# Performance work log

Hardware: AMD Instinct MI355X
Metric: run time of the kernel (lower is better)

Reference implementation:

```python
import jax, jax.numpy as jnp
import numpy as np

DIM = 2048
CTX_DIM = 4096
NUM_HEADS = 16
HEAD_DIM = DIM // NUM_HEADS
EPS = 1e-6


def _rms_norm(x, weight, eps=EPS):
    # RMSNorm over last dim with learned weight (native dtype path for fp32)
    var = jnp.mean(jnp.square(x), axis=-1, keepdims=True)
    return x * jax.lax.rsqrt(var + eps) * weight


def setup_inputs() -> dict:
    key = jax.random.key(0)
    ks = jax.random.split(key, 12)
    B, L, S = 1, 8192, 512
    sd_q = 1.0 / np.sqrt(DIM)
    sd_c = 1.0 / np.sqrt(CTX_DIM)
    return {
        "x": jax.random.normal(ks[0], (B, L, DIM), dtype=jnp.float32),
        "context": jax.random.normal(ks[1], (B, S, CTX_DIM), dtype=jnp.float32),
        "Wq": jax.random.normal(ks[2], (DIM, DIM), dtype=jnp.float32) * sd_q,
        "bq": jax.random.normal(ks[3], (DIM,), dtype=jnp.float32) * 0.01,
        "Wk": jax.random.normal(ks[4], (CTX_DIM, DIM), dtype=jnp.float32) * sd_c,
        "bk": jax.random.normal(ks[5], (DIM,), dtype=jnp.float32) * 0.01,
        "Wv": jax.random.normal(ks[6], (CTX_DIM, DIM), dtype=jnp.float32) * sd_c,
        "bv": jax.random.normal(ks[7], (DIM,), dtype=jnp.float32) * 0.01,
        "Wo": jax.random.normal(ks[8], (DIM, DIM), dtype=jnp.float32) * sd_q,
        "bo": jax.random.normal(ks[9], (DIM,), dtype=jnp.float32) * 0.01,
        "g_q": jnp.ones((DIM,), dtype=jnp.float32),
        "g_k": jnp.ones((DIM,), dtype=jnp.float32),
    }


def reference(x, context, Wq, bq, Wk, bk, Wv, bv, Wo, bo, g_q, g_k):
    B, L, C = x.shape
    S = context.shape[1]
    # QKV projections + RMSNorm on Q,K (over full model dim, pre head split)
    q = _rms_norm(x @ Wq + bq, g_q)           # [B, L, C]
    k = _rms_norm(context @ Wk + bk, g_k)     # [B, S, C]
    v = context @ Wv + bv                     # [B, S, C]
    # split heads
    q = q.reshape(B, L, NUM_HEADS, HEAD_DIM)
    k = k.reshape(B, S, NUM_HEADS, HEAD_DIM)
    v = v.reshape(B, S, NUM_HEADS, HEAD_DIM)
    # non-causal SDPA
    scale = 1.0 / np.sqrt(HEAD_DIM)
    scores = jnp.einsum("blhd,bshd->bhls", q, k) * scale
    probs = jax.nn.softmax(scores, axis=-1)
    attn = jnp.einsum("bhls,bshd->blhd", probs, v).reshape(B, L, C)
    return attn @ Wo + bo
```

## Files before the change

kernel.cpp:

```cpp
#include <hip/hip_runtime.h>
#include <hip/hip_bf16.h>
#include <stdint.h>

#define L_SEQ 8192
#define S_SEQ 512
#define DIM   2048
#define CTX   4096
#define NH    16
#define HD    128

typedef __bf16 bf16_t;
typedef bf16_t bf16x8 __attribute__((ext_vector_type(8)));
typedef float  f32x4_t __attribute__((ext_vector_type(4)));
typedef float  f32x16_t __attribute__((ext_vector_type(16)));

__device__ __forceinline__ ushort f2b(float f) {
  union { float f; uint32_t u; } v; v.f = f;
  uint32_t u = v.u;
  uint32_t r = (u + 0x7fffu + ((u >> 16) & 1u)) >> 16;
  return (ushort)r;
}
__device__ __forceinline__ uint32_t pk2(float a, float b) {
  return (uint32_t)f2b(a) | ((uint32_t)f2b(b) << 16);
}
__device__ __forceinline__ float b2f(ushort u) {
  union { uint32_t u; float f; } v; v.u = ((uint32_t)u) << 16;
  return v.f;
}
__device__ __forceinline__ void gll16(const ushort* g, ushort* l) {
  __builtin_amdgcn_global_load_lds((const __attribute__((address_space(1))) void*)g,
                                   (__attribute__((address_space(3))) void*)l, 16, 0, 0);
}

__global__ __launch_bounds__(256) void k_cast(const float* __restrict__ in,
                                              ushort* __restrict__ out) {
  const size_t i = ((size_t)blockIdx.x * 256 + threadIdx.x) * 8;
  float4 a = *(const float4*)(in + i);
  float4 b = *(const float4*)(in + i + 4);
  uint4 r;
  r.x = pk2(a.x, a.y); r.y = pk2(a.z, a.w);
  r.z = pk2(b.x, b.y); r.w = pk2(b.z, b.w);
  *(uint4*)(out + i) = r;
}

__global__ __launch_bounds__(256) void k_tcast(const float* __restrict__ src,
                                               ushort* __restrict__ dst, int K, int N) {
  __shared__ float t[32][33];
  int tx = threadIdx.x, ty = threadIdx.y;
  int n0 = blockIdx.x * 32, k0 = blockIdx.y * 32;
#pragma unroll
  for (int i = 0; i < 4; i++)
    t[ty + 8 * i][tx] = src[(size_t)(k0 + ty + 8 * i) * N + n0 + tx];
  __syncthreads();
#pragma unroll
  for (int i = 0; i < 4; i++)
    dst[(size_t)(n0 + ty + 8 * i) * K + k0 + tx] = f2b(t[tx][ty + 8 * i]);
}

__global__ __launch_bounds__(256) void k_rmsnorm(const ushort* __restrict__ in,
                                                 ushort* __restrict__ out,
                                                 const float* __restrict__ g, float scale) {
  const int row = blockIdx.x, tid = threadIdx.x;
  uint4 v = *(const uint4*)(in + (size_t)row * DIM + tid * 8);
  const uint32_t* vu = (const uint32_t*)&v;
  float f[8];
#pragma unroll
  for (int i = 0; i < 4; i++) {
    f[2 * i]     = b2f((ushort)(vu[i] & 0xffffu));
    f[2 * i + 1] = b2f((ushort)(vu[i] >> 16));
  }
  float s = 0.f;
#pragma unroll
  for (int i = 0; i < 8; i++) s += f[i] * f[i];
#pragma unroll
  for (int off = 32; off; off >>= 1) s += __shfl_down(s, off);
  __shared__ float wsum[4];
  __shared__ float rtot;
  if ((tid & 63) == 0) wsum[tid >> 6] = s;
  __syncthreads();
  if (tid == 0)
    rtot = rsqrtf((wsum[0] + wsum[1] + wsum[2] + wsum[3]) * (1.0f / DIM) + 1e-6f);
  __syncthreads();
  const float rms = rtot * scale;
  const float* gp = g + tid * 8;
  float4 g0 = *(const float4*)gp, g1 = *(const float4*)(gp + 4);
  ushort r[8];
  r[0] = f2b(f[0] * rms * g0.x); r[1] = f2b(f[1] * rms * g0.y);
  r[2] = f2b(f[2] * rms * g0.z); r[3] = f2b(f[3] * rms * g0.w);
  r[4] = f2b(f[4] * rms * g1.x); r[5] = f2b(f[5] * rms * g1.y);
  r[6] = f2b(f[6] * rms * g1.z); r[7] = f2b(f[7] * rms * g1.w);
  *(uint4*)(out + (size_t)row * DIM + tid * 8) = *(uint4*)r;
}

template <int OUT_MODE>
__global__ __launch_bounds__(512, 2) void k_gemm256(const ushort* __restrict__ A,
                                                    const ushort* __restrict__ Bt,
                                                    const float* __restrict__ bias,
                                                    void* __restrict__ outp,
                                                    int M, int N, int K) {
  __shared__ __align__(16) ushort lds[65536];
  const int tid = threadIdx.x;
  const int l = tid & 63, wid = tid >> 6;
  const int wm = wid >> 2, wn = wid & 3;
  const int lr = l & 15, lq = l >> 4;

  const int nwg = gridDim.x * gridDim.y;
  const int bid = blockIdx.y * gridDim.x + blockIdx.x;
  const int swz = (bid & 7) * (nwg >> 3) + (bid >> 3);
  const int m0 = (swz / gridDim.x) * 256, n0 = (swz % gridDim.x) * 256;

  f32x4_t acc[8][4];
#pragma unroll
  for (int i = 0; i < 8; i++)
#pragma unroll
    for (int j = 0; j < 4; j++) acc[i][j] = f32x4_t{0.f, 0.f, 0.f, 0.f};

  const int srow = l >> 3;
  const int schunk = ((l & 7) ^ (srow & 7)) * 8;
  auto stage = [&](int buf, int tile, int mat, int h) {
    const ushort* gp = mat ? Bt : A;
    const int rn0 = mat ? n0 : m0;
    const size_t r0 = (size_t)(rn0 + h * 128 + wid * 8 + srow);
    const ushort* g0 = gp + r0 * K + tile * 64 + schunk;
    ushort* l0 = &lds[buf * 32768 + mat * 16384 + (h * 128 + wid * 8) * 64];
    gll16(g0, l0);
    gll16(g0 + (size_t)64 * K, l0 + 64 * 64);
  };

  auto rdA = [&](int buf, int mf, int ks) -> bf16x8 {
    const int R = wm * 128 + mf * 16 + lr;
    return *(const bf16x8*)(&lds[buf * 32768 + R * 64 + (((ks * 4 + lq) ^ (R & 7)) * 8)]);
  };
  auto rdB = [&](int buf, int nf, int ks) -> bf16x8 {
    const int R = wn * 64 + nf * 16 + lr;
    return *(const bf16x8*)(&lds[buf * 32768 + 16384 + R * 64 + (((ks * 4 + lq) ^ (R & 7)) * 8)]);
  };

  const int NT = K >> 6;
  stage(0, 0, 0, 0); stage(0, 0, 0, 1); stage(0, 0, 1, 0); stage(0, 0, 1, 1);

  bf16x8 a[4][2], a2[4][2], b[2][2], b2[2][2];
  for (int kt = 0; kt < NT; kt++) {
    const int cur = kt & 1, nxt = cur ^ 1;
    const bool pf = (kt + 1 < NT);
    if (pf) { stage(nxt, kt + 1, 0, 0); asm volatile("s_waitcnt vmcnt(2)" ::: "memory"); }
    else    { asm volatile("s_waitcnt vmcnt(0)" ::: "memory"); }
    __builtin_amdgcn_sched_barrier(0);
    __builtin_amdgcn_s_barrier();
    __builtin_amdgcn_sched_barrier(0);
#pragma unroll
    for (int mf = 0; mf < 4; mf++) { a[mf][0] = rdA(cur, mf, 0); a[mf][1] = rdA(cur, mf, 1); }
#pragma unroll
    for (int nf = 0; nf < 2; nf++) { b[nf][0] = rdB(cur, nf, 0); b[nf][1] = rdB(cur, nf, 1); }
    __builtin_amdgcn_s_setprio(1);
#pragma unroll
    for (int mf = 0; mf < 4; mf++)
#pragma unroll
      for (int nf = 0; nf < 2; nf++) {
        acc[mf][nf] = __builtin_amdgcn_mfma_f32_16x16x32_bf16(a[mf][0], b[nf][0], acc[mf][nf], 0, 0, 0);
        acc[mf][nf] = __builtin_amdgcn_mfma_f32_16x16x32_bf16(a[mf][1], b[nf][1], acc[mf][nf], 0, 0, 0);
      }
    __builtin_amdgcn_s_setprio(0);
    __builtin_amdgcn_sched_barrier(0);
    __builtin_amdgcn_s_barrier();
    __builtin_amdgcn_sched_barrier(0);
#pragma unroll
    for (int mf = 0; mf < 4; mf++) { a2[mf][0] = rdA(cur, mf + 4, 0); a2[mf][1] = rdA(cur, mf + 4, 1); }
    if (pf) stage(nxt, kt + 1, 0, 1);
    __builtin_amdgcn_sched_barrier(0);
    __builtin_amdgcn_s_barrier();
    __builtin_amdgcn_sched_barrier(0);
    __builtin_amdgcn_s_setprio(1);
#pragma unroll
    for (int mf = 0; mf < 4; mf++)
#pragma unroll
      for (int nf = 0; nf < 2; nf++) {
        acc[mf + 4][nf] = __builtin_amdgcn_mfma_f32_16x16x32_bf16(a2[mf][0], b[nf][0], acc[mf + 4][nf], 0, 0, 0);
        acc[mf + 4][nf] = __builtin_amdgcn_mfma_f32_16x16x32_bf16(a2[mf][1], b[nf][1], acc[mf + 4][nf], 0, 0, 0);
      }
    __builtin_amdgcn_s_setprio(0);
    __builtin_amdgcn_sched_barrier(0);
    __builtin_amdgcn_s_barrier();
    __builtin_amdgcn_sched_barrier(0);
#pragma unroll
    for (int nf = 0; nf < 2; nf++) { b2[nf][0] = rdB(cur, nf + 2, 0); b2[nf][1] = rdB(cur, nf + 2, 1); }
    if (pf) stage(nxt, kt + 1, 1, 0);
    __builtin_amdgcn_sched_barrier(0);
    __builtin_amdgcn_s_barrier();
    __builtin_amdgcn_sched_barrier(0);
    __builtin_amdgcn_s_setprio(1);
#pragma unroll
    for (int mf = 0; mf < 4; mf++)
#pragma unroll
      for (int nf = 0; nf < 2; nf++) {
        acc[mf + 4][nf + 2] = __builtin_amdgcn_mfma_f32_16x16x32_bf16(a2[mf][0], b2[nf][0], acc[mf + 4][nf + 2], 0, 0, 0);
        acc[mf + 4][nf + 2] = __builtin_amdgcn_mfma_f32_16x16x32_bf16(a2[mf][1], b2[nf][1], acc[mf + 4][nf + 2], 0, 0, 0);
      }
    __builtin_amdgcn_s_setprio(0);
    __builtin_amdgcn_sched_barrier(0);
    __builtin_amdgcn_s_barrier();
    __builtin_amdgcn_sched_barrier(0);
#pragma unroll
    for (int mf = 0; mf < 4; mf++) { a[mf][0] = rdA(cur, mf, 0); a[mf][1] = rdA(cur, mf, 1); }
    if (pf) stage(nxt, kt + 1, 1, 1);
    __builtin_amdgcn_sched_barrier(0);
    __builtin_amdgcn_s_barrier();
    __builtin_amdgcn_sched_barrier(0);
    __builtin_amdgcn_s_setprio(1);
#pragma unroll
    for (int mf = 0; mf < 4; mf++)
#pragma unroll
      for (int nf = 0; nf < 2; nf++) {
        acc[mf][nf + 2] = __builtin_amdgcn_mfma_f32_16x16x32_bf16(a[mf][0], b2[nf][0], acc[mf][nf + 2], 0, 0, 0);
        acc[mf][nf + 2] = __builtin_amdgcn_mfma_f32_16x16x32_bf16(a[mf][1], b2[nf][1], acc[mf][nf + 2], 0, 0, 0);
      }
    __builtin_amdgcn_s_setprio(0);
    __builtin_amdgcn_sched_barrier(0);
    __builtin_amdgcn_s_barrier();
    __builtin_amdgcn_sched_barrier(0);
  }

#pragma unroll
  for (int nf = 0; nf < 4; nf++) {
    const int col = n0 + wn * 64 + nf * 16 + lr;
    const float bv = bias[col];
#pragma unroll
    for (int mf = 0; mf < 8; mf++) {
#pragma unroll
      for (int r = 0; r < 4; r++) {
        const int row = m0 + wm * 128 + mf * 16 + lq * 4 + r;
        const float v = acc[mf][nf][r] + bv;
        if constexpr (OUT_MODE == 0)
          ((float*)outp)[(size_t)row * N + col] = v;
        else
          ((ushort*)outp)[(size_t)row * N + col] = f2b(v);
      }
    }
  }
}

template <int OUT_MODE>
__global__ __launch_bounds__(256) void k_gemm_bt(const ushort* __restrict__ A,
                                                 const ushort* __restrict__ Bt,
                                                 const float* __restrict__ bias,
                                                 const float* __restrict__ bias2,
                                                 void* __restrict__ outp,
                                                 void* __restrict__ outp2,
                                                 int M, int N, int K) {
  __shared__ __align__(16) ushort As[2 * 128 * 32];
  __shared__ __align__(16) ushort Bs[2 * 128 * 32];
  const int tid = threadIdx.x;
  const int l = tid & 63, wid = tid >> 6;
  const int wr = wid >> 1, wc = wid & 1;
  const int lr = l & 15, lq = l >> 4;

  const int nwg = gridDim.x * gridDim.y;
  const int bid = blockIdx.y * gridDim.x + blockIdx.x;
  const int swz = (bid & 7) * (nwg >> 3) + (bid >> 3);
  const int m0 = (swz / gridDim.x) * 128, n0 = (swz % gridDim.x) * 128;

  f32x4_t acc[4][4];
#pragma unroll
  for (int i = 0; i < 4; i++)
#pragma unroll
    for (int j = 0; j < 4; j++) acc[i][j] = f32x4_t{0.f, 0.f, 0.f, 0.f};

  const int srow = l >> 2;
  const int scol = (l & 3) * 8;
  const ushort* ga0 = A  + (size_t)(m0 + wid * 16 + srow) * K + scol;
  const ushort* ga1 = A  + (size_t)(m0 + (4 + wid) * 16 + srow) * K + scol;
  const ushort* gb0 = Bt + (size_t)(n0 + wid * 16 + srow) * K + scol;
  const ushort* gb1 = Bt + (size_t)(n0 + (4 + wid) * 16 + srow) * K + scol;

  auto stageAB = [&](int buf, int kt) {
    const int ko = kt * 32;
    gll16(ga0 + ko, &As[buf * 4096 + wid * 512]);
    gll16(ga1 + ko, &As[buf * 4096 + (4 + wid) * 512]);
    gll16(gb0 + ko, &Bs[buf * 4096 + wid * 512]);
    gll16(gb1 + ko, &Bs[buf * 4096 + (4 + wid) * 512]);
  };

  const int NT = K >> 5;
  stageAB(0, 0);
  for (int kt = 0; kt < NT; kt++) {
    const int cur = kt & 1;
    const bool pf = (kt + 1 < NT);
    if (pf) { stageAB(cur ^ 1, kt + 1); asm volatile("s_waitcnt vmcnt(4)" ::: "memory"); }
    else    { asm volatile("s_waitcnt vmcnt(0)" ::: "memory"); }
    __builtin_amdgcn_sched_barrier(0);
    __builtin_amdgcn_s_barrier();
    __builtin_amdgcn_sched_barrier(0);

    bf16x8 af[4], bfr[4];
#pragma unroll
    for (int mi = 0; mi < 4; mi++)
      af[mi] = *(const bf16x8*)(&As[cur * 4096 + (wr * 64 + mi * 16 + lr) * 32 + lq * 8]);
#pragma unroll
    for (int ni = 0; ni < 4; ni++)
      bfr[ni] = *(const bf16x8*)(&Bs[cur * 4096 + (wc * 64 + ni * 16 + lr) * 32 + lq * 8]);
#pragma unroll
    for (int mi = 0; mi < 4; mi++)
#pragma unroll
      for (int ni = 0; ni < 4; ni++)
        acc[mi][ni] = __builtin_amdgcn_mfma_f32_16x16x32_bf16(af[mi], bfr[ni], acc[mi][ni], 0, 0, 0);
    __builtin_amdgcn_sched_barrier(0);
    __builtin_amdgcn_s_barrier();
    __builtin_amdgcn_sched_barrier(0);
  }

#pragma unroll
  for (int mi = 0; mi < 4; mi++) {
#pragma unroll
    for (int ni = 0; ni < 4; ni++) {
      const int col = n0 + wc * 64 + ni * 16 + lr;
      float bv;
      if constexpr (OUT_MODE == 3) bv = (col < DIM) ? bias[col] : bias2[col - DIM];
      else bv = bias[col];
#pragma unroll
      for (int r = 0; r < 4; r++) {
        const int row = m0 + wr * 64 + mi * 16 + lq * 4 + r;
        const float v = acc[mi][ni][r] + bv;
        if constexpr (OUT_MODE == 0)
          ((float*)outp)[(size_t)row * N + col] = v;
        else if constexpr (OUT_MODE == 1)
          ((ushort*)outp)[(size_t)row * N + col] = f2b(v);
        else {
          if (col < DIM) ((ushort*)outp)[(size_t)row * DIM + col] = f2b(v);
          else ((ushort*)outp2)[(size_t)(col - DIM) * M + row] = f2b(v);
        }
      }
    }
  }
}

__global__ __launch_bounds__(256) void k_attn(const ushort* __restrict__ Qb,
                                              const ushort* __restrict__ Kb,
                                              const ushort* __restrict__ Vt,
                                              ushort* __restrict__ Ob) {
  __shared__ __align__(16) ushort smem[16384];
  ushort* Ks = smem;
  ushort* Vs = smem + 64 * 128;

  const int tid = threadIdx.x;
  const int l = tid & 63, wid = tid >> 6;
  const int lo = l & 31, hi = l >> 5;

  const int bid = blockIdx.x;
  const int swz = (bid & 7) * 128 + (bid >> 3);
  const int h = swz >> 6;
  const int q0 = (swz & 63) * 128 + wid * 32;

  bf16x8 qf[8];
  {
    const ushort* qp = Qb + (size_t)(q0 + lo) * DIM + h * HD + hi * 8;
#pragma unroll
    for (int ds = 0; ds < 8; ds++) qf[ds] = *(const bf16x8*)(qp + ds * 16);
  }

  f32x16_t o[4] = {};
  float m_run = -1e30f, l_run = 0.f;

  for (int kvb = 0; kvb < S_SEQ / 64; kvb++) {
    __syncthreads();
#pragma unroll
    for (int i = 0; i < 4; i++) {
      const int c = i * 256 + tid, row = c >> 4, cs = c & 15;
      gll16(Kb + (size_t)(kvb * 64 + row) * DIM + h * HD + ((cs ^ (row & 7)) * 8),
            Ks + c * 8);
    }
#pragma unroll
    for (int i = 0; i < 4; i++) {
      const int c = i * 256 + tid, row = c >> 3, cs = c & 7;
      gll16(Vt + (size_t)(h * HD + row) * S_SEQ + kvb * 64 + ((cs ^ (row & 7)) * 8),
            Vs + c * 8);
    }
    __syncthreads();

    f32x16_t sA = {}, sB = {};
#pragma unroll
    for (int ds = 0; ds < 8; ds++) {
      const int ch = ((hi + ds * 2) ^ (lo & 7)) * 8;
      bf16x8 kA = *(const bf16x8*)(Ks + lo * 128 + ch);
      bf16x8 kB = *(const bf16x8*)(Ks + (32 + lo) * 128 + ch);
      sA = __builtin_amdgcn_mfma_f32_32x32x16_bf16(kA, qf[ds], sA, 0, 0, 0);
      sB = __builtin_amdgcn_mfma_f32_32x32x16_bf16(kB, qf[ds], sB, 0, 0, 0);
    }

    float p[32];
#pragma unroll
    for (int i = 0; i < 16; i++) { p[i] = sA[i]; p[16 + i] = sB[i]; }
    float pm = p[0];
#pragma unroll
    for (int i = 1; i < 32; i++) pm = fmaxf(pm, p[i]);
    pm = fmaxf(pm, __shfl_xor(pm, 32));
    const float mn = fmaxf(m_run, pm);
    const float corr = __expf(m_run - mn);
    m_run = mn;
    float ps = 0.f;
#pragma unroll
    for (int i = 0; i < 32; i++) { p[i] = __expf(p[i] - mn); ps += p[i]; }
    ps += __shfl_xor(ps, 32);
    l_run = l_run * corr + ps;
#pragma unroll
    for (int nt = 0; nt < 4; nt++) o[nt] *= corr;

    uint32_t c[16];
#pragma unroll
    for (int j = 0; j < 16; j++) c[j] = pk2(p[2 * j], p[2 * j + 1]);
    bf16x8 pf[4];
#pragma unroll
    for (int s = 0; s < 4; s++) {
      const uint32_t ca = c[4 * s], cb = c[4 * s + 1], cc = c[4 * s + 2], cd = c[4 * s + 3];
      const uint32_t sa = __shfl_xor(ca, 32), sb = __shfl_xor(cb, 32);
      const uint32_t sc = __shfl_xor(cc, 32), sd = __shfl_xor(cd, 32);
      union { uint32_t u[4]; bf16x8 v; } f;
      f.u[0] = hi ? sc : ca; f.u[1] = hi ? sd : cb;
      f.u[2] = hi ? cc : sa; f.u[3] = hi ? cd : sb;
      pf[s] = f.v;
    }

#pragma unroll
    for (int nt = 0; nt < 4; nt++) {
      const int vrow = nt * 32 + lo;
#pragma unroll
      for (int s = 0; s < 4; s++) {
        bf16x8 vf = *(const bf16x8*)(Vs + vrow * 64 + (((s * 2 + hi) ^ (lo & 7)) * 8));
        o[nt] = __builtin_amdgcn_mfma_f32_32x32x16_bf16(vf, pf[s], o[nt], 0, 0, 0);
      }
    }
  }

  const float inv = 1.0f / l_run;
#pragma unroll
  for (int nt = 0; nt < 4; nt++) o[nt] *= inv;

  __syncthreads();
  float* tb = (float*)smem + wid * (32 * 33);
  const int q2 = l >> 1, dh = (l & 1) * 16;
#pragma unroll
  for (int nt = 0; nt < 4; nt++) {
#pragma unroll
    for (int r = 0; r < 16; r++)
      tb[lo * 33 + ((r & 3) + 8 * (r >> 2) + 4 * hi)] = o[nt][r];
    asm volatile("s_waitcnt lgkmcnt(0)" ::: "memory");
    __builtin_amdgcn_sched_barrier(0);
    ushort tmp[16];
#pragma unroll
    for (int j = 0; j < 16; j++) tmp[j] = f2b(tb[q2 * 33 + dh + j]);
    asm volatile("s_waitcnt lgkmcnt(0)" ::: "memory");
    __builtin_amdgcn_sched_barrier(0);
    const size_t oaddr = (size_t)(q0 + q2) * DIM + h * HD + nt * 32 + dh;
    *(uint4*)(Ob + oaddr) = *(uint4*)tmp;
    *(uint4*)(Ob + oaddr + 8) = *(uint4*)(tmp + 8);
  }
}

extern "C" void kernel_launch(void* const* d_in, const int* in_sizes, int n_in,
                              void* d_out, int out_size, void* d_ws, size_t ws_size,
                              hipStream_t stream) {
  const float* x   = (const float*)d_in[0];
  const float* ctx = (const float*)d_in[1];
  const float* Wq  = (const float*)d_in[2];
  const float* bq  = (const float*)d_in[3];
  const float* Wk  = (const float*)d_in[4];
  const float* bk  = (const float*)d_in[5];
  const float* Wv  = (const float*)d_in[6];
  const float* bv  = (const float*)d_in[7];
  const float* Wo  = (const float*)d_in[8];
  const float* bo  = (const float*)d_in[9];
  const float* gq  = (const float*)d_in[10];
  const float* gk  = (const float*)d_in[11];

  char* ws = (char*)d_ws;
  ushort* wqt   = (ushort*)(ws);
  ushort* wkt   = (ushort*)(ws + 8388608);
  ushort* wvt   = (ushort*)(ws + 25165824);
  ushort* wot   = (ushort*)(ws + 41943040);
  ushort* qb    = (ushort*)(ws + 50331648);
  ushort* kb    = (ushort*)(ws + 83886080);
  ushort* vt    = (ushort*)(ws + 85983232);
  ushort* xb    = (ushort*)(ws + 88080384);
  ushort* ctxb  = (ushort*)(ws + 88080384);
  ushort* qraw  = (ushort*)(ws + 121634816);
  ushort* kraw  = (ushort*)(ws + 121634816);
  ushort* attnb = (ushort*)(ws + 121634816);

  k_cast<<<L_SEQ * DIM / 8 / 256, 256, 0, stream>>>(x, xb);
  k_tcast<<<dim3(DIM / 32, DIM / 32), dim3(32, 8), 0, stream>>>(Wq, wqt, DIM, DIM);
  k_tcast<<<dim3(DIM / 32, CTX / 32), dim3(32, 8), 0, stream>>>(Wk, wkt, CTX, DIM);
  k_tcast<<<dim3(DIM / 32, CTX / 32), dim3(32, 8), 0, stream>>>(Wv, wvt, CTX, DIM);
  k_tcast<<<dim3(DIM / 32, DIM / 32), dim3(32, 8), 0, stream>>>(Wo, wot, DIM, DIM);

  k_gemm256<1><<<dim3(DIM / 256, L_SEQ / 256), 512, 0, stream>>>(xb, wqt, bq, qraw, L_SEQ, DIM, DIM);
  k_cast<<<S_SEQ * CTX / 8 / 256, 256, 0, stream>>>(ctx, ctxb);
  k_rmsnorm<<<L_SEQ, 256, 0, stream>>>(qraw, qb, gq, 0.08838834764831843f);
  k_gemm_bt<3><<<dim3(2 * DIM / 128, S_SEQ / 128), 256, 0, stream>>>(ctxb, wkt, bk, bv, kraw, vt, S_SEQ, 2 * DIM, CTX);
  k_rmsnorm<<<S_SEQ, 256, 0, stream>>>(kraw, kb, gk, 1.0f);
  k_attn<<<L_SEQ / 128 * NH, 256, 0, stream>>>(qb, kb, vt, attnb);
  k_gemm256<0><<<dim3(DIM / 256, L_SEQ / 256), 512, 0, stream>>>(attnb, wot, bo, d_out, L_SEQ, DIM, DIM);
}
```

Measured before the change: 355.5 us.

## Specialize KV projection GEMM with 128x64 tiles, 4-stage pipeline, swizzled LDS

```diff
diff --git a/kernel.cpp b/kernel.cpp
--- a/kernel.cpp
+++ b/kernel.cpp
@@ -239,70 +239,74 @@
   }
 }
 
-template <int OUT_MODE>
-__global__ __launch_bounds__(256) void k_gemm_bt(const ushort* __restrict__ A,
-                                                 const ushort* __restrict__ Bt,
-                                                 const float* __restrict__ bias,
-                                                 const float* __restrict__ bias2,
-                                                 void* __restrict__ outp,
-                                                 void* __restrict__ outp2,
-                                                 int M, int N, int K) {
-  __shared__ __align__(16) ushort As[2 * 128 * 32];
-  __shared__ __align__(16) ushort Bs[2 * 128 * 32];
+__global__ __launch_bounds__(256) void k_gemmkv(const ushort* __restrict__ A,
+                                                const ushort* __restrict__ Bt,
+                                                const float* __restrict__ biasK,
+                                                const float* __restrict__ biasV,
+                                                ushort* __restrict__ outK,
+                                                ushort* __restrict__ outVt) {
+  __shared__ __align__(16) ushort As[4][128 * 32];
+  __shared__ __align__(16) ushort Bs[4][64 * 32];
   const int tid = threadIdx.x;
   const int l = tid & 63, wid = tid >> 6;
   const int wr = wid >> 1, wc = wid & 1;
   const int lr = l & 15, lq = l >> 4;
-
-  const int nwg = gridDim.x * gridDim.y;
-  const int bid = blockIdx.y * gridDim.x + blockIdx.x;
-  const int swz = (bid & 7) * (nwg >> 3) + (bid >> 3);
-  const int m0 = (swz / gridDim.x) * 128, n0 = (swz % gridDim.x) * 128;
-
-  f32x4_t acc[4][4];
+  const int K = CTX, M = S_SEQ;
+
+  const int bid = blockIdx.x;
+  const int swz = (bid & 7) * 32 + (bid >> 3);
+  const int n0 = (swz >> 2) * 64, m0 = (swz & 3) * 128;
+
+  f32x4_t acc[4][2];
 #pragma unroll
   for (int i = 0; i < 4; i++)
 #pragma unroll
-    for (int j = 0; j < 4; j++) acc[i][j] = f32x4_t{0.f, 0.f, 0.f, 0.f};
+    for (int j = 0; j < 2; j++) acc[i][j] = f32x4_t{0.f, 0.f, 0.f, 0.f};
 
   const int srow = l >> 2;
-  const int scol = (l & 3) * 8;
-  const ushort* ga0 = A  + (size_t)(m0 + wid * 16 + srow) * K + scol;
-  const ushort* ga1 = A  + (size_t)(m0 + (4 + wid) * 16 + srow) * K + scol;
-  const ushort* gb0 = Bt + (size_t)(n0 + wid * 16 + srow) * K + scol;
-  const ushort* gb1 = Bt + (size_t)(n0 + (4 + wid) * 16 + srow) * K + scol;
-
-  auto stageAB = [&](int buf, int kt) {
+  const int schunk = ((l & 3) ^ ((srow >> 1) & 3)) * 8;
+  const ushort* gA = A  + (size_t)(m0 + srow) * K + schunk;
+  const ushort* gB = Bt + (size_t)(n0 + wid * 16 + srow) * K + schunk;
+
+  auto stage = [&](int buf, int kt) {
     const int ko = kt * 32;
-    gll16(ga0 + ko, &As[buf * 4096 + wid * 512]);
-    gll16(ga1 + ko, &As[buf * 4096 + (4 + wid) * 512]);
-    gll16(gb0 + ko, &Bs[buf * 4096 + wid * 512]);
-    gll16(gb1 + ko, &Bs[buf * 4096 + (4 + wid) * 512]);
+    gll16(gA + (size_t)(wid * 16) * K + ko,      &As[buf][(wid * 16) * 32]);
+    gll16(gA + (size_t)(64 + wid * 16) * K + ko, &As[buf][(64 + wid * 16) * 32]);
+    gll16(gB + ko,                               &Bs[buf][(wid * 16) * 32]);
+  };
+  auto rdA = [&](int buf, int mi) -> bf16x8 {
+    const int R = wr * 64 + mi * 16 + lr;
+    return *(const bf16x8*)(&As[buf][R * 32 + ((lq ^ ((R >> 1) & 3)) * 8)]);
+  };
+  auto rdB = [&](int buf, int ni) -> bf16x8 {
+    const int R = wc * 32 + ni * 16 + lr;
+    return *(const bf16x8*)(&Bs[buf][R * 32 + ((lq ^ ((R >> 1) & 3)) * 8)]);
   };
 
   const int NT = K >> 5;
-  stageAB(0, 0);
-  for (int kt = 0; kt < NT; kt++) {
-    const int cur = kt & 1;
-    const bool pf = (kt + 1 < NT);
-    if (pf) { stageAB(cur ^ 1, kt + 1); asm volatile("s_waitcnt vmcnt(4)" ::: "memory"); }
-    else    { asm volatile("s_waitcnt vmcnt(0)" ::: "memory"); }
-    __builtin_amdgcn_sched_barrier(0);
-    __builtin_amdgcn_s_barrier();
-    __builtin_amdgcn_sched_barrier(0);
-
-    bf16x8 af[4], bfr[4];
+  stage(0, 0); stage(1, 1); stage(2, 2);
+  for (int t = 0; t < NT; t++) {
+    const int cur = t & 3;
+    if (t + 3 < NT) { stage((t + 3) & 3, t + 3); asm volatile("s_waitcnt vmcnt(9)" ::: "memory"); }
+    else if (t + 2 < NT) { asm volatile("s_waitcnt vmcnt(6)" ::: "memory"); }
+    else if (t + 1 < NT) { asm volatile("s_waitcnt vmcnt(3)" ::: "memory"); }
+    else                 { asm volatile("s_waitcnt vmcnt(0)" ::: "memory"); }
+    __builtin_amdgcn_sched_barrier(0);
+    __builtin_amdgcn_s_barrier();
+    __builtin_amdgcn_sched_barrier(0);
+
+    bf16x8 af[4], bfr[2];
+#pragma unroll
+    for (int mi = 0; mi < 4; mi++) af[mi] = rdA(cur, mi);
+#pragma unroll
+    for (int ni = 0; ni < 2; ni++) bfr[ni] = rdB(cur, ni);
+    __builtin_amdgcn_s_setprio(1);
 #pragma unroll
     for (int mi = 0; mi < 4; mi++)
-      af[mi] = *(const bf16x8*)(&As[cur * 4096 + (wr * 64 + mi * 16 + lr) * 32 + lq * 8]);
-#pragma unroll
-    for (int ni = 0; ni < 4; ni++)
-      bfr[ni] = *(const bf16x8*)(&Bs[cur * 4096 + (wc * 64 + ni * 16 + lr) * 32 + lq * 8]);
-#pragma unroll
-    for (int mi = 0; mi < 4; mi++)
-#pragma unroll
-      for (int ni = 0; ni < 4; ni++)
+#pragma unroll
+      for (int ni = 0; ni < 2; ni++)
         acc[mi][ni] = __builtin_amdgcn_mfma_f32_16x16x32_bf16(af[mi], bfr[ni], acc[mi][ni], 0, 0, 0);
+    __builtin_amdgcn_s_setprio(0);
     __builtin_amdgcn_sched_barrier(0);
     __builtin_amdgcn_s_barrier();
     __builtin_amdgcn_sched_barrier(0);
@@ -311,23 +315,15 @@
 #pragma unroll
   for (int mi = 0; mi < 4; mi++) {
 #pragma unroll
-    for (int ni = 0; ni < 4; ni++) {
-      const int col = n0 + wc * 64 + ni * 16 + lr;
-      float bv;
-      if constexpr (OUT_MODE == 3) bv = (col < DIM) ? bias[col] : bias2[col - DIM];
-      else bv = bias[col];
+    for (int ni = 0; ni < 2; ni++) {
+      const int col = n0 + wc * 32 + ni * 16 + lr;
+      const float bv = (col < DIM) ? biasK[col] : biasV[col - DIM];
 #pragma unroll
       for (int r = 0; r < 4; r++) {
         const int row = m0 + wr * 64 + mi * 16 + lq * 4 + r;
         const float v = acc[mi][ni][r] + bv;
-        if constexpr (OUT_MODE == 0)
-          ((float*)outp)[(size_t)row * N + col] = v;
-        else if constexpr (OUT_MODE == 1)
-          ((ushort*)outp)[(size_t)row * N + col] = f2b(v);
-        else {
-          if (col < DIM) ((ushort*)outp)[(size_t)row * DIM + col] = f2b(v);
-          else ((ushort*)outp2)[(size_t)(col - DIM) * M + row] = f2b(v);
-        }
+        if (col < DIM) outK[(size_t)row * DIM + col] = f2b(v);
+        else           outVt[(size_t)(col - DIM) * M + row] = f2b(v);
       }
     }
   }
@@ -494,7 +490,7 @@
   k_gemm256<1><<<dim3(DIM / 256, L_SEQ / 256), 512, 0, stream>>>(xb, wqt, bq, qraw, L_SEQ, DIM, DIM);
   k_cast<<<S_SEQ * CTX / 8 / 256, 256, 0, stream>>>(ctx, ctxb);
   k_rmsnorm<<<L_SEQ, 256, 0, stream>>>(qraw, qb, gq, 0.08838834764831843f);
-  k_gemm_bt<3><<<dim3(2 * DIM / 128, S_SEQ / 128), 256, 0, stream>>>(ctxb, wkt, bk, bv, kraw, vt, S_SEQ, 2 * DIM, CTX);
+  k_gemmkv<<<256, 256, 0, stream>>>(ctxb, wkt, bk, bv, kraw, vt);
   k_rmsnorm<<<S_SEQ, 256, 0, stream>>>(kraw, kb, gk, 1.0f);
   k_attn<<<L_SEQ / 128 * NH, 256, 0, stream>>>(qb, kb, vt, attnb);
   k_gemm256<0><<<dim3(DIM / 256, L_SEQ / 256), 512, 0, stream>>>(attnb, wot, bo, d_out, L_SEQ, DIM, DIM);
```

Measured after the change: 337.5 us. -5.0%, faster.
